# Optimization experiments

Hardware: AMD Instinct MI355X
Metric: run time of the kernel (lower is better)

Reference implementation:

```python
import jax, jax.numpy as jnp
import numpy as np

N, E = 50000, 800000
IN, HID, OUT = 256, 128, 64


def setup_inputs() -> dict:
    key = jax.random.key(0)
    ks = jax.random.split(key, 8)
    x = jax.random.normal(ks[0], (N, IN), dtype=jnp.float32)
    edge_index = jax.random.randint(ks[1], (2, E), 0, N, dtype=jnp.int64)
    # PyG GCNConv: Linear weight [out, in] (glorot-ish), bias [out] (zeros init; use small randn for a nontrivial baseline)
    W1 = jax.random.normal(ks[2], (HID, IN), dtype=jnp.float32) / np.sqrt(IN)
    b1 = jax.random.normal(ks[3], (HID,), dtype=jnp.float32) * 0.01
    Wmu = jax.random.normal(ks[4], (OUT, HID), dtype=jnp.float32) / np.sqrt(HID)
    bmu = jax.random.normal(ks[5], (OUT,), dtype=jnp.float32) * 0.01
    Wlv = jax.random.normal(ks[6], (OUT, HID), dtype=jnp.float32) / np.sqrt(HID)
    blv = jax.random.normal(ks[7], (OUT,), dtype=jnp.float32) * 0.01
    return {"x": x, "edge_index": edge_index, "W1": W1, "b1": b1,
            "Wmu": Wmu, "bmu": bmu, "Wlv": Wlv, "blv": blv}


def reference(x, edge_index, W1, b1, Wmu, bmu, Wlv, blv):
    n = x.shape[0]
    loop = jnp.arange(n, dtype=edge_index.dtype)
    src = jnp.concatenate([edge_index[0], loop])  # [E+N]
    dst = jnp.concatenate([edge_index[1], loop])
    # symmetric normalization with self-loops: deg computed on destinations
    deg = jax.ops.segment_sum(jnp.ones_like(dst, dtype=x.dtype), dst, num_segments=n)
    dis = jax.lax.rsqrt(deg)  # deg >= 1 due to self-loops
    norm = dis[src] * dis[dst]  # [E+N]

    def gcn(h, W, b):
        hw = h @ W.T                                   # [N, out]
        msg = hw[src] * norm[:, None]                  # [E+N, out] gather + scale
        return jax.ops.segment_sum(msg, dst, num_segments=n) + b

    h = jax.nn.relu(gcn(x, W1, b1))
    # dropout(p=0.5) is identity in eval mode
    return (gcn(h, Wmu, bmu), gcn(h, Wlv, blv))
```

## Files before the change

kernel.cpp:

```cpp
#include <hip/hip_runtime.h>

#define N_NODES 50000
#define N_EDGES 800000
#define DIN 256
#define DHID 128
#define DOUT 64
#define NB_SCAN 49
#define SENT N_NODES

typedef __attribute__((ext_vector_type(8))) short short8;
typedef __attribute__((ext_vector_type(4))) float f32x4;

static __device__ __forceinline__ short f2bf(float f) {
    union { float f; unsigned u; } v; v.f = f;
    unsigned r = v.u + 0x7FFFu + ((v.u >> 16) & 1u);
    return (short)(r >> 16);
}
static __device__ __forceinline__ float bflo(unsigned p) {
    union { unsigned u; float f; } v; v.u = p << 16; return v.f;
}
static __device__ __forceinline__ float bfhi(unsigned p) {
    union { unsigned u; float f; } v; v.u = p & 0xFFFF0000u; return v.f;
}


__global__ void count_kernel(const int* __restrict__ ei, int* __restrict__ cnt,
                             int* __restrict__ loc) {
    int stride = gridDim.x * blockDim.x;
    for (int e = blockIdx.x * blockDim.x + threadIdx.x; e < N_EDGES; e += stride) {
        loc[e] = atomicAdd(&cnt[ei[N_EDGES + e]], 1);
    }
}

__global__ __launch_bounds__(1024) void bsum_kernel(const int* __restrict__ cnt,
                                                    int* __restrict__ bsum) {
    __shared__ int ws[16];
    int tid = threadIdx.x, i = blockIdx.x * 1024 + tid;
    int v = (i < N_NODES) ? cnt[i] : 0;
    v = (v + 7) & ~7;
    #pragma unroll
    for (int off = 32; off >= 1; off >>= 1) v += __shfl_xor(v, off);
    if ((tid & 63) == 0) ws[tid >> 6] = v;
    __syncthreads();
    if (tid == 0) {
        int s = 0;
        #pragma unroll
        for (int w = 0; w < 16; ++w) s += ws[w];
        bsum[blockIdx.x] = s;
    }
}

__global__ void bscan_kernel(const int* __restrict__ bsum, int* __restrict__ bo,
                             int* __restrict__ rowptr) {
    int l = threadIdx.x;
    int v = (l < NB_SCAN) ? bsum[l] : 0;
    int x = v;
    #pragma unroll
    for (int off = 1; off < 64; off <<= 1) {
        int y = __shfl_up(x, off);
        if (l >= off) x += y;
    }
    if (l < NB_SCAN) bo[l] = x - v;
    if (l == 63) rowptr[N_NODES] = x;
}

__global__ __launch_bounds__(1024) void scan_apply_kernel(const int* __restrict__ cnt,
        const int* __restrict__ bo, int* __restrict__ rowptr,
        float* __restrict__ dis, int* __restrict__ col) {
    __shared__ int wsum[16];
    int tid = threadIdx.x, i = blockIdx.x * 1024 + tid;
    int lane = tid & 63, wid = tid >> 6;
    int v = (i < N_NODES) ? cnt[i] : 0;
    int p = (v + 7) & ~7;
    int x = p;
    #pragma unroll
    for (int off = 1; off < 64; off <<= 1) {
        int y = __shfl_up(x, off);
        if (lane >= off) x += y;
    }
    if (lane == 63) wsum[wid] = x;
    __syncthreads();
    if (tid == 0) {
        int s = 0;
        #pragma unroll
        for (int w = 0; w < 16; ++w) { int t = wsum[w]; wsum[w] = s; s += t; }
    }
    __syncthreads();
    int excl = bo[blockIdx.x] + wsum[wid] + (x - p);
    if (i < N_NODES) {
        rowptr[i] = excl;
        dis[i] = rsqrtf((float)(v + 1));
        for (int q = v; q < p; ++q) col[excl + q] = SENT;
    }
}

__global__ void fill_kernel(const int* __restrict__ ei, const int* __restrict__ loc,
                            const int* __restrict__ rowptr, int* __restrict__ col) {
    int stride = gridDim.x * blockDim.x;
    for (int e = blockIdx.x * blockDim.x + threadIdx.x; e < N_EDGES; e += stride) {
        int s = ei[e];
        int d = ei[N_EDGES + e];
        col[rowptr[d] + loc[e]] = s;
    }
}


__global__ void wprep_kernel(const float* __restrict__ W1, const float* __restrict__ Wmu,
                             const float* __restrict__ Wlv, short* __restrict__ W1b,
                             short* __restrict__ Wctb) {
    int tid = blockIdx.x * blockDim.x + threadIdx.x;
    if (tid < DHID * DIN) {
        W1b[tid] = f2bf(W1[tid]);
    } else if (tid < DHID * DIN + 2 * DOUT * DHID) {
        int t = tid - DHID * DIN;
        Wctb[t] = f2bf((t < DOUT * DHID) ? Wmu[t] : Wlv[t - DOUT * DHID]);
    }
}


__global__ __launch_bounds__(256) void xprep_kernel(const float* __restrict__ x,
        const float* __restrict__ dis, short* __restrict__ xb) {
    const int total = N_NODES * (DIN / 8);
    int stride = gridDim.x * blockDim.x;
    for (int c = blockIdx.x * blockDim.x + threadIdx.x; c < total; c += stride) {
        int row = c >> 5;
        float d = dis[row];
        const float* src = x + (size_t)c * 8;
        float4 f0 = *(const float4*)src;
        float4 f1 = *(const float4*)(src + 4);
        short8 o;
        o[0] = f2bf(f0.x * d); o[1] = f2bf(f0.y * d);
        o[2] = f2bf(f0.z * d); o[3] = f2bf(f0.w * d);
        o[4] = f2bf(f1.x * d); o[5] = f2bf(f1.y * d);
        o[6] = f2bf(f1.z * d); o[7] = f2bf(f1.w * d);
        *(short8*)(xb + (size_t)c * 8) = o;
    }
}


__global__ __launch_bounds__(256) void gemm1_mfma_kernel(const short* __restrict__ xb,
        const short* __restrict__ W1b, short* __restrict__ u1b) {
    const int lane = threadIdx.x & 63, w = threadIdx.x >> 6;
    const int l15 = lane & 15, kg = lane >> 4;
    const int rowg = w >> 1, colh = w & 1;
    const int nb = blockIdx.x * 32 + rowg * 16;
    const int r0 = nb + l15;
    const bool valid = r0 < N_NODES;
    const short* arow = xb + (size_t)r0 * DIN;

    f32x4 acc[4] = {};
    #pragma unroll
    for (int ks = 0; ks < 8; ++ks) {
        const int k0 = ks * 32 + kg * 8;
        short8 a = valid ? *(const short8*)(arow + k0)
                         : short8{0, 0, 0, 0, 0, 0, 0, 0};
        #pragma unroll
        for (int c = 0; c < 4; ++c) {
            const int cc = colh * 4 + c;
            short8 b = *(const short8*)(W1b + (size_t)(cc * 16 + l15) * DIN + k0);
            acc[c] = __builtin_amdgcn_mfma_f32_16x16x32_bf16(a, b, acc[c], 0, 0, 0);
        }
    }

    const int rb = nb + kg * 4;
    #pragma unroll
    for (int c = 0; c < 4; ++c) {
        const int j = (colh * 4 + c) * 16 + l15;
        #pragma unroll
        for (int e = 0; e < 4; ++e) {
            int r = rb + e;
            if (r < N_NODES)
                u1b[(size_t)r * DHID + j] = f2bf(acc[c][e]);
        }
    }
}


template <bool LAYER1>
__global__ __launch_bounds__(256) void pull_kernel(const int* __restrict__ rowptr,
        const int* __restrict__ col, const short* __restrict__ uin,
        const float* __restrict__ dis, const float* __restrict__ b1,
        unsigned* __restrict__ uout) {
    const int wid = threadIdx.x >> 6, lane = threadIdx.x & 63;
    const int i = blockIdx.x * 4 + wid;
    if (i >= N_NODES) return;
    const int beg = rowptr[i], end = rowptr[i + 1];
    const unsigned* __restrict__ up = (const unsigned*)uin;
    float ax = 0.f, ay = 0.f;
    for (int base = beg; base < end; base += 64) {
        const int rem = end - base;
        const int m = rem < 64 ? rem : 64;
        int cv = (lane < m) ? col[base + lane] : SENT;
        for (int t = 0; t < m; t += 8) {
            int c0 = __shfl(cv, t);
            int c1 = __shfl(cv, t + 1);
            int c2 = __shfl(cv, t + 2);
            int c3 = __shfl(cv, t + 3);
            int c4 = __shfl(cv, t + 4);
            int c5 = __shfl(cv, t + 5);
            int c6 = __shfl(cv, t + 6);
            int c7 = __shfl(cv, t + 7);
            unsigned v0 = up[(size_t)c0 * 64 + lane];
            unsigned v1 = up[(size_t)c1 * 64 + lane];
            unsigned v2 = up[(size_t)c2 * 64 + lane];
            unsigned v3 = up[(size_t)c3 * 64 + lane];
            unsigned v4 = up[(size_t)c4 * 64 + lane];
            unsigned v5 = up[(size_t)c5 * 64 + lane];
            unsigned v6 = up[(size_t)c6 * 64 + lane];
            unsigned v7 = up[(size_t)c7 * 64 + lane];
            ax += bflo(v0); ay += bfhi(v0);
            ax += bflo(v1); ay += bfhi(v1);
            ax += bflo(v2); ay += bfhi(v2);
            ax += bflo(v3); ay += bfhi(v3);
            ax += bflo(v4); ay += bfhi(v4);
            ax += bflo(v5); ay += bfhi(v5);
            ax += bflo(v6); ay += bfhi(v6);
            ax += bflo(v7); ay += bfhi(v7);
        }
    }
    const float di = dis[i];
    const unsigned sv = up[(size_t)i * 64 + lane];
    float tx = di * (ax + bflo(sv));
    float ty = di * (ay + bfhi(sv));
    if (LAYER1) {
        float2 b = *(const float2*)(b1 + lane * 2);
        tx = fmaxf(tx + b.x, 0.f) * di;
        ty = fmaxf(ty + b.y, 0.f) * di;
    }
    unsigned o = ((unsigned)(unsigned short)f2bf(tx)) |
                 (((unsigned)(unsigned short)f2bf(ty)) << 16);
    uout[(size_t)i * 64 + lane] = o;
}


__global__ __launch_bounds__(256) void gemm2_mfma_kernel(const short* __restrict__ a2b,
        const short* __restrict__ Wctb, const float* __restrict__ bmu,
        const float* __restrict__ blv, float* __restrict__ out) {
    const int lane = threadIdx.x & 63, w = threadIdx.x >> 6;
    const int l15 = lane & 15, kg = lane >> 4;
    const int nb = blockIdx.x * 64;
    const int r0 = nb + w * 16 + l15;
    const bool valid = r0 < N_NODES;
    const short* arow = a2b + (size_t)r0 * DHID;

    f32x4 acc[8] = {};
    #pragma unroll
    for (int ks = 0; ks < 4; ++ks) {
        const int k0 = ks * 32 + kg * 8;
        short8 a = valid ? *(const short8*)(arow + k0)
                         : short8{0, 0, 0, 0, 0, 0, 0, 0};
        #pragma unroll
        for (int c = 0; c < 8; ++c) {
            short8 b = *(const short8*)(Wctb + (size_t)(c * 16 + l15) * DHID + k0);
            acc[c] = __builtin_amdgcn_mfma_f32_16x16x32_bf16(a, b, acc[c], 0, 0, 0);
        }
    }

    float bias[8];
    #pragma unroll
    for (int c = 0; c < 8; ++c) {
        int j = c * 16 + l15;
        bias[c] = (j < DOUT) ? bmu[j] : blv[j - DOUT];
    }
    const int rb = nb + w * 16 + kg * 4;
    #pragma unroll
    for (int c = 0; c < 8; ++c) {
        const int j = c * 16 + l15;
        float* dst = (j < DOUT) ? (out + j)
                                : (out + (size_t)N_NODES * DOUT + (j - DOUT));
        #pragma unroll
        for (int e = 0; e < 4; ++e) {
            int r = rb + e;
            if (r < N_NODES)
                dst[(size_t)r * DOUT] = acc[c][e] + bias[c];
        }
    }
}


extern "C" void kernel_launch(void* const* d_in, const int* in_sizes, int n_in,
                              void* d_out, int out_size, void* d_ws, size_t ws_size,
                              hipStream_t stream) {
    const float* x   = (const float*)d_in[0];
    const int*   ei  = (const int*)d_in[1];
    const float* W1  = (const float*)d_in[2];
    const float* b1  = (const float*)d_in[3];
    const float* Wmu = (const float*)d_in[4];
    const float* bmu = (const float*)d_in[5];
    const float* Wlv = (const float*)d_in[6];
    const float* blv = (const float*)d_in[7];
    float* out = (float*)d_out;

    char* ws = (char*)d_ws;
    size_t off = 0;
    auto alloc = [&](size_t bytes) -> char* {
        char* p = ws + off;
        off += (bytes + 255) & ~(size_t)255;
        return p;
    };
    const size_t COL_CAP = (size_t)N_EDGES + 8 * (size_t)N_NODES + 64;
    int*   cnt    = (int*)  alloc((size_t)N_NODES * 4);
    int*   rowptr = (int*)  alloc((size_t)(N_NODES + 1) * 4);
    float* dis    = (float*)alloc((size_t)N_NODES * 4);
    int*   loc    = (int*)  alloc((size_t)N_EDGES * 4);
    int*   col    = (int*)  alloc(COL_CAP * 4);
    int*   bsum   = (int*)  alloc((size_t)NB_SCAN * 4);
    int*   bo     = (int*)  alloc((size_t)NB_SCAN * 4);
    short* W1b    = (short*)alloc((size_t)DHID * DIN * 2);
    short* Wctb   = (short*)alloc((size_t)2 * DOUT * DHID * 2);
    short* xb     = (short*)alloc((size_t)N_NODES * DIN * 2);
    short* u1b    = (short*)alloc((size_t)(N_NODES + 1) * DHID * 2);
    short* u2b    = (short*)alloc((size_t)(N_NODES + 1) * DHID * 2);
    short* a2b    = u1b;

    hipMemsetAsync(cnt, 0, (size_t)N_NODES * 4, stream);
    hipMemsetAsync(u1b + (size_t)N_NODES * DHID, 0, DHID * 2, stream);
    hipMemsetAsync(u2b + (size_t)N_NODES * DHID, 0, DHID * 2, stream);
    wprep_kernel<<<192, 256, 0, stream>>>(W1, Wmu, Wlv, W1b, Wctb);
    count_kernel<<<1024, 256, 0, stream>>>(ei, cnt, loc);
    bsum_kernel<<<NB_SCAN, 1024, 0, stream>>>(cnt, bsum);
    bscan_kernel<<<1, 64, 0, stream>>>(bsum, bo, rowptr);
    scan_apply_kernel<<<NB_SCAN, 1024, 0, stream>>>(cnt, bo, rowptr, dis, col);
    fill_kernel<<<1024, 256, 0, stream>>>(ei, loc, rowptr, col);
    xprep_kernel<<<2048, 256, 0, stream>>>(x, dis, xb);
    gemm1_mfma_kernel<<<(N_NODES + 31) / 32, 256, 0, stream>>>(xb, W1b, u1b);
    pull_kernel<true><<<N_NODES / 4, 256, 0, stream>>>(rowptr, col, u1b, dis, b1,
                                                       (unsigned*)u2b);
    pull_kernel<false><<<N_NODES / 4, 256, 0, stream>>>(rowptr, col, u2b, dis, nullptr,
                                                        (unsigned*)a2b);
    gemm2_mfma_kernel<<<(N_NODES + 63) / 64, 256, 0, stream>>>(a2b, Wctb, bmu, blv, out);
}
```

Baseline: 284.0 us.

## Vectorize pull gathers to 16-byte loads and widen gemm1 tiles per warp

The pull kernel now has each 16-lane group fetch a full neighbour row with uint4 loads, so four neighbours are handled per load instruction. Partial sums are then combined across groups with xor shuffles and only one group writes the output. The idea is to cut the number of memory instructions in the latency-bound gather. Separately, gemm1 now computes all 128 output columns per warp over 64-row blocks, reusing the A fragment, and the sentinel-row memsets are folded into wprep to save two launches. The costs are more registers and a cross-lane reduction per node.

```diff
diff --git a/kernel.cpp b/kernel.cpp
--- a/kernel.cpp
+++ b/kernel.cpp
@@ -21,6 +21,10 @@
 }
 static __device__ __forceinline__ float bfhi(unsigned p) {
     union { unsigned u; float f; } v; v.u = p & 0xFFFF0000u; return v.f;
+}
+static __device__ __forceinline__ unsigned pk(float lo, float hi) {
+    return ((unsigned)(unsigned short)f2bf(lo)) |
+           (((unsigned)(unsigned short)f2bf(hi)) << 16);
 }
 
 
@@ -107,13 +111,18 @@
 
 __global__ void wprep_kernel(const float* __restrict__ W1, const float* __restrict__ Wmu,
                              const float* __restrict__ Wlv, short* __restrict__ W1b,
-                             short* __restrict__ Wctb) {
+                             short* __restrict__ Wctb, short* __restrict__ u1b,
+                             short* __restrict__ u2b) {
     int tid = blockIdx.x * blockDim.x + threadIdx.x;
     if (tid < DHID * DIN) {
         W1b[tid] = f2bf(W1[tid]);
     } else if (tid < DHID * DIN + 2 * DOUT * DHID) {
         int t = tid - DHID * DIN;
         Wctb[t] = f2bf((t < DOUT * DHID) ? Wmu[t] : Wlv[t - DOUT * DHID]);
+    } else if (tid < DHID * DIN + 2 * DOUT * DHID + DHID) {
+        int t = tid - (DHID * DIN + 2 * DOUT * DHID);
+        u1b[(size_t)SENT * DHID + t] = 0;
+        u2b[(size_t)SENT * DHID + t] = 0;
     }
 }
 
@@ -142,30 +151,28 @@
         const short* __restrict__ W1b, short* __restrict__ u1b) {
     const int lane = threadIdx.x & 63, w = threadIdx.x >> 6;
     const int l15 = lane & 15, kg = lane >> 4;
-    const int rowg = w >> 1, colh = w & 1;
-    const int nb = blockIdx.x * 32 + rowg * 16;
-    const int r0 = nb + l15;
+    const int nb = blockIdx.x * 64;
+    const int r0 = nb + w * 16 + l15;
     const bool valid = r0 < N_NODES;
     const short* arow = xb + (size_t)r0 * DIN;
 
-    f32x4 acc[4] = {};
+    f32x4 acc[8] = {};
     #pragma unroll
     for (int ks = 0; ks < 8; ++ks) {
         const int k0 = ks * 32 + kg * 8;
         short8 a = valid ? *(const short8*)(arow + k0)
                          : short8{0, 0, 0, 0, 0, 0, 0, 0};
         #pragma unroll
-        for (int c = 0; c < 4; ++c) {
-            const int cc = colh * 4 + c;
-            short8 b = *(const short8*)(W1b + (size_t)(cc * 16 + l15) * DIN + k0);
+        for (int c = 0; c < 8; ++c) {
+            short8 b = *(const short8*)(W1b + (size_t)(c * 16 + l15) * DIN + k0);
             acc[c] = __builtin_amdgcn_mfma_f32_16x16x32_bf16(a, b, acc[c], 0, 0, 0);
         }
     }
 
-    const int rb = nb + kg * 4;
-    #pragma unroll
-    for (int c = 0; c < 4; ++c) {
-        const int j = (colh * 4 + c) * 16 + l15;
+    const int rb = nb + w * 16 + kg * 4;
+    #pragma unroll
+    for (int c = 0; c < 8; ++c) {
+        const int j = c * 16 + l15;
         #pragma unroll
         for (int e = 0; e < 4; ++e) {
             int r = rb + e;
@@ -182,54 +189,71 @@
         const float* __restrict__ dis, const float* __restrict__ b1,
         unsigned* __restrict__ uout) {
     const int wid = threadIdx.x >> 6, lane = threadIdx.x & 63;
+    const int g = lane >> 4, j = lane & 15;
     const int i = blockIdx.x * 4 + wid;
     if (i >= N_NODES) return;
     const int beg = rowptr[i], end = rowptr[i + 1];
-    const unsigned* __restrict__ up = (const unsigned*)uin;
-    float ax = 0.f, ay = 0.f;
+    const uint4* __restrict__ up4 = (const uint4*)uin;
+    float a0 = 0.f, a1 = 0.f, a2 = 0.f, a3 = 0.f;
+    float a4 = 0.f, a5 = 0.f, a6 = 0.f, a7 = 0.f;
     for (int base = beg; base < end; base += 64) {
         const int rem = end - base;
         const int m = rem < 64 ? rem : 64;
         int cv = (lane < m) ? col[base + lane] : SENT;
         for (int t = 0; t < m; t += 8) {
-            int c0 = __shfl(cv, t);
-            int c1 = __shfl(cv, t + 1);
-            int c2 = __shfl(cv, t + 2);
-            int c3 = __shfl(cv, t + 3);
-            int c4 = __shfl(cv, t + 4);
-            int c5 = __shfl(cv, t + 5);
-            int c6 = __shfl(cv, t + 6);
-            int c7 = __shfl(cv, t + 7);
-            unsigned v0 = up[(size_t)c0 * 64 + lane];
-            unsigned v1 = up[(size_t)c1 * 64 + lane];
-            unsigned v2 = up[(size_t)c2 * 64 + lane];
-            unsigned v3 = up[(size_t)c3 * 64 + lane];
-            unsigned v4 = up[(size_t)c4 * 64 + lane];
-            unsigned v5 = up[(size_t)c5 * 64 + lane];
-            unsigned v6 = up[(size_t)c6 * 64 + lane];
-            unsigned v7 = up[(size_t)c7 * 64 + lane];
-            ax += bflo(v0); ay += bfhi(v0);
-            ax += bflo(v1); ay += bfhi(v1);
-            ax += bflo(v2); ay += bfhi(v2);
-            ax += bflo(v3); ay += bfhi(v3);
-            ax += bflo(v4); ay += bfhi(v4);
-            ax += bflo(v5); ay += bfhi(v5);
-            ax += bflo(v6); ay += bfhi(v6);
-            ax += bflo(v7); ay += bfhi(v7);
-        }
-    }
+            int c0 = __shfl(cv, t + g);
+            int c1 = __shfl(cv, t + 4 + g);
+            uint4 v0 = up4[(size_t)c0 * 16 + j];
+            uint4 v1 = up4[(size_t)c1 * 16 + j];
+            a0 += bflo(v0.x); a1 += bfhi(v0.x);
+            a2 += bflo(v0.y); a3 += bfhi(v0.y);
+            a4 += bflo(v0.z); a5 += bfhi(v0.z);
+            a6 += bflo(v0.w); a7 += bfhi(v0.w);
+            a0 += bflo(v1.x); a1 += bfhi(v1.x);
+            a2 += bflo(v1.y); a3 += bfhi(v1.y);
+            a4 += bflo(v1.z); a5 += bfhi(v1.z);
+            a6 += bflo(v1.w); a7 += bfhi(v1.w);
+        }
+    }
+    a0 += __shfl_xor(a0, 16); a0 += __shfl_xor(a0, 32);
+    a1 += __shfl_xor(a1, 16); a1 += __shfl_xor(a1, 32);
+    a2 += __shfl_xor(a2, 16); a2 += __shfl_xor(a2, 32);
+    a3 += __shfl_xor(a3, 16); a3 += __shfl_xor(a3, 32);
+    a4 += __shfl_xor(a4, 16); a4 += __shfl_xor(a4, 32);
+    a5 += __shfl_xor(a5, 16); a5 += __shfl_xor(a5, 32);
+    a6 += __shfl_xor(a6, 16); a6 += __shfl_xor(a6, 32);
+    a7 += __shfl_xor(a7, 16); a7 += __shfl_xor(a7, 32);
+
+    const uint4 sv = up4[(size_t)i * 16 + j];
     const float di = dis[i];
-    const unsigned sv = up[(size_t)i * 64 + lane];
-    float tx = di * (ax + bflo(sv));
-    float ty = di * (ay + bfhi(sv));
+    float t0 = di * (a0 + bflo(sv.x));
+    float t1 = di * (a1 + bfhi(sv.x));
+    float t2 = di * (a2 + bflo(sv.y));
+    float t3 = di * (a3 + bfhi(sv.y));
+    float t4 = di * (a4 + bflo(sv.z));
+    float t5 = di * (a5 + bfhi(sv.z));
+    float t6 = di * (a6 + bflo(sv.w));
+    float t7 = di * (a7 + bfhi(sv.w));
     if (LAYER1) {
-        float2 b = *(const float2*)(b1 + lane * 2);
-        tx = fmaxf(tx + b.x, 0.f) * di;
-        ty = fmaxf(ty + b.y, 0.f) * di;
-    }
-    unsigned o = ((unsigned)(unsigned short)f2bf(tx)) |
-                 (((unsigned)(unsigned short)f2bf(ty)) << 16);
-    uout[(size_t)i * 64 + lane] = o;
+        float4 bl = *(const float4*)(b1 + j * 8);
+        float4 bh = *(const float4*)(b1 + j * 8 + 4);
+        t0 = fmaxf(t0 + bl.x, 0.f) * di;
+        t1 = fmaxf(t1 + bl.y, 0.f) * di;
+        t2 = fmaxf(t2 + bl.z, 0.f) * di;
+        t3 = fmaxf(t3 + bl.w, 0.f) * di;
+        t4 = fmaxf(t4 + bh.x, 0.f) * di;
+        t5 = fmaxf(t5 + bh.y, 0.f) * di;
+        t6 = fmaxf(t6 + bh.z, 0.f) * di;
+        t7 = fmaxf(t7 + bh.w, 0.f) * di;
+    }
+    if (g == 0) {
+        uint4 o;
+        o.x = pk(t0, t1);
+        o.y = pk(t2, t3);
+        o.z = pk(t4, t5);
+        o.w = pk(t6, t7);
+        ((uint4*)uout)[(size_t)i * 16 + j] = o;
+    }
 }
 
 
@@ -314,16 +338,14 @@
     short* a2b    = u1b;
 
     hipMemsetAsync(cnt, 0, (size_t)N_NODES * 4, stream);
-    hipMemsetAsync(u1b + (size_t)N_NODES * DHID, 0, DHID * 2, stream);
-    hipMemsetAsync(u2b + (size_t)N_NODES * DHID, 0, DHID * 2, stream);
-    wprep_kernel<<<192, 256, 0, stream>>>(W1, Wmu, Wlv, W1b, Wctb);
+    wprep_kernel<<<193, 256, 0, stream>>>(W1, Wmu, Wlv, W1b, Wctb, u1b, u2b);
     count_kernel<<<1024, 256, 0, stream>>>(ei, cnt, loc);
     bsum_kernel<<<NB_SCAN, 1024, 0, stream>>>(cnt, bsum);
     bscan_kernel<<<1, 64, 0, stream>>>(bsum, bo, rowptr);
     scan_apply_kernel<<<NB_SCAN, 1024, 0, stream>>>(cnt, bo, rowptr, dis, col);
     fill_kernel<<<1024, 256, 0, stream>>>(ei, loc, rowptr, col);
     xprep_kernel<<<2048, 256, 0, stream>>>(x, dis, xb);
-    gemm1_mfma_kernel<<<(N_NODES + 31) / 32, 256, 0, stream>>>(xb, W1b, u1b);
+    gemm1_mfma_kernel<<<(N_NODES + 63) / 64, 256, 0, stream>>>(xb, W1b, u1b);
     pull_kernel<true><<<N_NODES / 4, 256, 0, stream>>>(rowptr, col, u1b, dis, b1,
                                                        (unsigned*)u2b);
     pull_kernel<false><<<N_NODES / 4, 256, 0, stream>>>(rowptr, col, u2b, dis, nullptr,
```

Measured after the change: 282.8 us. No clear change (-0.4%).
